# Optimization experiments

Measured on AMD Instinct MI355X. Metric: run time of the kernel, lower is better.

## Reference

```python
import jax, jax.numpy as jnp
import numpy as np

EMB_DIM = 1024
N_HEADS = 16
HEAD_DIM = EMB_DIM // N_HEADS


def setup_inputs() -> dict:
    key = jax.random.key(0)
    ks = jax.random.split(key, 6)
    B, S, D = 2, 2048, EMB_DIM
    s = 1.0 / np.sqrt(D)
    return {
        "x": jax.random.normal(ks[0], (B, S, D), dtype=jnp.float32),
        "wq": jax.random.normal(ks[1], (D, D), dtype=jnp.float32) * s,
        "wk": jax.random.normal(ks[2], (D, D), dtype=jnp.float32) * s,
        "wv": jax.random.normal(ks[3], (D, D), dtype=jnp.float32) * s,
        "wo": jax.random.normal(ks[4], (D, D), dtype=jnp.float32) * s,
        "bo": jax.random.normal(ks[5], (D,), dtype=jnp.float32) * 0.01,
    }


def reference(x, wq, wk, wv, wo, bo):
    B, S, D = x.shape
    H, Hd = N_HEADS, HEAD_DIM
    # projections (torch Linear: y = x @ W.T; here weights are stored as [in, out])
    q = (x @ wq).reshape(B, S, H, Hd).transpose(0, 2, 1, 3)  # [B,H,S,Hd]
    k = (x @ wk).reshape(B, S, H, Hd).transpose(0, 2, 1, 3)
    v = (x @ wv).reshape(B, S, H, Hd).transpose(0, 2, 1, 3)
    scores = jnp.einsum("bhqd,bhkd->bhqk", q, k)  # [B,H,S,S]
    causal = jnp.tril(jnp.ones((S, S), dtype=bool))  # keep lower triangle
    scores = jnp.where(causal, scores, -jnp.inf)
    weights = jax.nn.softmax(scores / np.sqrt(Hd), axis=-1)
    ctx = jnp.einsum("bhqk,bhkd->bhqd", weights, v)  # [B,H,S,Hd]
    ctx = ctx.transpose(0, 2, 1, 3).reshape(B, S, D)
    return ctx @ wo + bo
```

## Files before the change

### kernel.cpp

```cpp
#include <hip/hip_runtime.h>
#include <hip/hip_bf16.h>

constexpr int B = 2, S = 2048, D = 1024, H = 16, Hd = 64;
constexpr int M = B * S;
constexpr int K = 1024;

typedef __attribute__((ext_vector_type(8))) short short8;
typedef __attribute__((ext_vector_type(4))) float f32x4;

__device__ __forceinline__ float bf2f(unsigned short u) {
    return __uint_as_float(((unsigned)u) << 16);
}
__device__ __forceinline__ unsigned short f2bf(float f) {
    unsigned u = __float_as_uint(f);
    u += 0x7FFF + ((u >> 16) & 1);
    return (unsigned short)(u >> 16);
}
__device__ __forceinline__ void gload_lds16(const unsigned short* g, unsigned short* l) {
    __builtin_amdgcn_global_load_lds(
        (const __attribute__((address_space(1))) void*)g,
        (__attribute__((address_space(3))) void*)l, 16, 0, 0);
}

__global__ __launch_bounds__(256) void convert_x_kernel(
    const float* __restrict__ x, unsigned short* __restrict__ xb)
{
    const size_t i = ((size_t)blockIdx.x * 256 + threadIdx.x) * 8;
    float4 a = *(const float4*)(x + i), b = *(const float4*)(x + i + 4);
    ushort4 u0 = {f2bf(a.x), f2bf(a.y), f2bf(a.z), f2bf(a.w)};
    ushort4 u1 = {f2bf(b.x), f2bf(b.y), f2bf(b.z), f2bf(b.w)};
    *(ushort4*)(xb + i) = u0;
    *(ushort4*)(xb + i + 4) = u1;
}

__global__ __launch_bounds__(256) void transpose_w_kernel(
    const float* __restrict__ wq, const float* __restrict__ wk,
    const float* __restrict__ wv, const float* __restrict__ wo,
    unsigned short* __restrict__ wqkv_t, unsigned short* __restrict__ wo_t)
{
    __shared__ float tile[64][65];
    const int z = blockIdx.z;
    const float* w = (z == 0) ? wq : (z == 1) ? wk : (z == 2) ? wv : wo;
    unsigned short* dst = (z == 3) ? wo_t : wqkv_t + (size_t)z * K * K;
    const int k0 = blockIdx.x * 64, n0 = blockIdx.y * 64;
    const int t = threadIdx.x;
    #pragma unroll
    for (int it = 0; it < 16; ++it) {
        int idx = t + it * 256;
        tile[idx >> 6][idx & 63] = w[(size_t)(k0 + (idx >> 6)) * K + n0 + (idx & 63)];
    }
    __syncthreads();
    #pragma unroll
    for (int it = 0; it < 16; ++it) {
        int idx = t + it * 256;
        int r = idx >> 6, c = idx & 63;
        dst[(size_t)(n0 + r) * K + k0 + c] = f2bf(tile[c][r]);
    }
}

__global__ __launch_bounds__(256) void qkv_mfma_kernel(
    const unsigned short* __restrict__ xa, const unsigned short* __restrict__ bt,
    unsigned short* __restrict__ q, unsigned short* __restrict__ k,
    unsigned short* __restrict__ vt)
{
    __shared__ unsigned short A_lds[128][32];
    __shared__ unsigned short B_lds[128][32];
    const int t = threadIdx.x, w = t >> 6, l = t & 63;
    const int lr = l & 15, lg = l >> 4;
    const int wm = w >> 1, wn = w & 1;
    const int m0 = blockIdx.x * 128, n0 = blockIdx.y * 128;
    const int srow = l >> 2, skofs = (l & 3) * 8;

    f32x4 acc[4][4];
    #pragma unroll
    for (int i = 0; i < 4; ++i)
        #pragma unroll
        for (int j = 0; j < 4; ++j) acc[i][j] = (f32x4){0.f, 0.f, 0.f, 0.f};

    for (int k0 = 0; k0 < K; k0 += 32) {
        #pragma unroll
        for (int p = 0; p < 2; ++p) {
            const int c = w * 2 + p;
            gload_lds16(xa + (size_t)(m0 + c * 16 + srow) * K + k0 + skofs, &A_lds[c * 16][0]);
            gload_lds16(bt + (size_t)(n0 + c * 16 + srow) * K + k0 + skofs, &B_lds[c * 16][0]);
        }
        __syncthreads();
        short8 af[4], bf[4];
        #pragma unroll
        for (int i = 0; i < 4; ++i) af[i] = *(const short8*)&A_lds[wm * 64 + i * 16 + lr][lg * 8];
        #pragma unroll
        for (int j = 0; j < 4; ++j) bf[j] = *(const short8*)&B_lds[wn * 64 + j * 16 + lr][lg * 8];
        #pragma unroll
        for (int i = 0; i < 4; ++i)
            #pragma unroll
            for (int j = 0; j < 4; ++j)
                acc[i][j] = __builtin_amdgcn_mfma_f32_16x16x32_bf16(af[i], bf[j], acc[i][j], 0, 0, 0);
        __syncthreads();
    }

    const int z = (n0 >> 10);
    const float scale = (z == 0) ? 0.125f * 1.44269504f : 1.0f;
    #pragma unroll
    for (int i = 0; i < 4; ++i) {
        const int mbase = m0 + wm * 64 + i * 16 + lg * 4;
        #pragma unroll
        for (int j = 0; j < 4; ++j) {
            const int n = n0 + wn * 64 + j * 16 + lr;
            const int nn = n & 1023, hh = nn >> 6, hd = nn & 63;
            #pragma unroll
            for (int r = 0; r < 4; ++r) {
                const int mm = mbase + r, bb = mm >> 11, ss = mm & (S - 1);
                const unsigned short val = f2bf(acc[i][j][r] * scale);
                if (z == 0)      q[((size_t)(bb * H + hh) * S + ss) * Hd + hd] = val;
                else if (z == 1) k[((size_t)(bb * H + hh) * S + ss) * Hd + hd] = val;
                else             vt[((size_t)(bb * H + hh) * Hd + hd) * S + ss] = val;
            }
        }
    }
}

__global__ __launch_bounds__(256) void out_mfma_kernel(
    const unsigned short* __restrict__ a, const unsigned short* __restrict__ bt,
    const float* __restrict__ bias, float* __restrict__ out)
{
    __shared__ unsigned short A_lds[128][32];
    __shared__ unsigned short B_lds[128][32];
    const int t = threadIdx.x, w = t >> 6, l = t & 63;
    const int lr = l & 15, lg = l >> 4;
    const int wm = w >> 1, wn = w & 1;
    const int m0 = blockIdx.x * 128, n0 = blockIdx.y * 128;
    const int srow = l >> 2, skofs = (l & 3) * 8;

    f32x4 acc[4][4];
    #pragma unroll
    for (int i = 0; i < 4; ++i)
        #pragma unroll
        for (int j = 0; j < 4; ++j) acc[i][j] = (f32x4){0.f, 0.f, 0.f, 0.f};

    for (int k0 = 0; k0 < K; k0 += 32) {
        #pragma unroll
        for (int p = 0; p < 2; ++p) {
            const int c = w * 2 + p;
            gload_lds16(a  + (size_t)(m0 + c * 16 + srow) * K + k0 + skofs, &A_lds[c * 16][0]);
            gload_lds16(bt + (size_t)(n0 + c * 16 + srow) * K + k0 + skofs, &B_lds[c * 16][0]);
        }
        __syncthreads();
        short8 af[4], bf[4];
        #pragma unroll
        for (int i = 0; i < 4; ++i) af[i] = *(const short8*)&A_lds[wm * 64 + i * 16 + lr][lg * 8];
        #pragma unroll
        for (int j = 0; j < 4; ++j) bf[j] = *(const short8*)&B_lds[wn * 64 + j * 16 + lr][lg * 8];
        #pragma unroll
        for (int i = 0; i < 4; ++i)
            #pragma unroll
            for (int j = 0; j < 4; ++j)
                acc[i][j] = __builtin_amdgcn_mfma_f32_16x16x32_bf16(af[i], bf[j], acc[i][j], 0, 0, 0);
        __syncthreads();
    }

    #pragma unroll
    for (int i = 0; i < 4; ++i) {
        const int mbase = m0 + wm * 64 + i * 16 + lg * 4;
        #pragma unroll
        for (int j = 0; j < 4; ++j) {
            const int n = n0 + wn * 64 + j * 16 + lr;
            const float bv = bias[n];
            #pragma unroll
            for (int r = 0; r < 4; ++r)
                out[(size_t)(mbase + r) * D + n] = acc[i][j][r] + bv;
        }
    }
}

__global__ __launch_bounds__(256) void attn_mfma_kernel(
    const unsigned short* __restrict__ q, const unsigned short* __restrict__ k,
    const unsigned short* __restrict__ vt, unsigned short* __restrict__ ctx)
{
    __shared__ unsigned short Kb[64 * 64];
    __shared__ unsigned short Vb[64 * 64];
    __shared__ unsigned short P_lds[4][16][72];
    const int t = threadIdx.x, w = t >> 6, l = t & 63;
    const int lr = l & 15, lg = l >> 4;
    const int hh = blockIdx.y, bb = blockIdx.z;
    const int qt = ((int)blockIdx.x + 5 * (int)blockIdx.y + 16 * (int)blockIdx.z) & 31;
    const int q0 = qt * 64 + w * 16;
    const int diag = qt;
    const size_t base  = (size_t)(bb * H + hh) * S * Hd;
    const size_t vbase = (size_t)(bb * H + hh) * Hd * S;

    const int srow0 = w * 16 + (l >> 3);
    const int scol  = (l & 7) * 8;

    short8 qf[2];
    #pragma unroll
    for (int c = 0; c < 2; ++c)
        qf[c] = *(const short8*)(q + base + (size_t)(q0 + lr) * Hd + c * 32 + lg * 8);

    f32x4 accO[4];
    #pragma unroll
    for (int hb = 0; hb < 4; ++hb) accO[hb] = (f32x4){0.f, 0.f, 0.f, 0.f};
    float m_run = -INFINITY, l_run = 0.f;

    {
        short8 k0r[2], v0r[2];
        #pragma unroll
        for (int it = 0; it < 2; ++it) {
            const int row = srow0 + it * 8;
            k0r[it] = *(const short8*)(k + base + (size_t)row * Hd + scol);
            v0r[it] = *(const short8*)(vt + vbase + (size_t)row * S + scol);
        }
        #pragma unroll
        for (int it = 0; it < 2; ++it) {
            const int row = srow0 + it * 8;
            const int wc = (scol ^ ((row & 7) * 8));
            *(short8*)&Kb[row * 64 + wc] = k0r[it];
            *(short8*)&Vb[row * 64 + wc] = v0r[it];
        }
    }
    __syncthreads();

    for (int kt = 0; kt <= diag; ++kt) {
        short8 nK[2], nV[2];
        if (kt < diag) {
            const unsigned short* kg = k + base + (size_t)(kt + 1) * 64 * Hd;
            const unsigned short* vg = vt + vbase + (size_t)(kt + 1) * 64;
            #pragma unroll
            for (int it = 0; it < 2; ++it) {
                const int row = srow0 + it * 8;
                nK[it] = *(const short8*)(kg + (size_t)row * Hd + scol);
                nV[it] = *(const short8*)(vg + (size_t)row * S + scol);
            }
        }

        f32x4 accS[4];
        __builtin_amdgcn_s_setprio(1);
        #pragma unroll
        for (int kc = 0; kc < 4; ++kc) {
            accS[kc] = (f32x4){0.f, 0.f, 0.f, 0.f};
            const int krow = kc * 16 + lr;
            #pragma unroll
            for (int c = 0; c < 2; ++c) {
                short8 kf = *(const short8*)&Kb[krow * 64 +
                    ((c * 32 + lg * 8) ^ ((krow & 7) * 8))];
                accS[kc] = __builtin_amdgcn_mfma_f32_16x16x32_bf16(kf, qf[c], accS[kc], 0, 0, 0);
            }
        }
        __builtin_amdgcn_s_setprio(0);

        float ps[16];
        #pragma unroll
        for (int kc = 0; kc < 4; ++kc)
            #pragma unroll
            for (int r = 0; r < 4; ++r) {
                float s = accS[kc][r];
                if (kt == diag && (kc * 16 + lg * 4 + r > w * 16 + lr)) s = -INFINITY;
                ps[kc * 4 + r] = s;
            }
        float m8[8];
        #pragma unroll
        for (int i = 0; i < 8; ++i) m8[i] = fmaxf(ps[i], ps[i + 8]);
        float m4a = fmaxf(m8[0], m8[4]), m4b = fmaxf(m8[1], m8[5]);
        float m4c = fmaxf(m8[2], m8[6]), m4d = fmaxf(m8[3], m8[7]);
        float mloc = fmaxf(fmaxf(m4a, m4b), fmaxf(m4c, m4d));
        mloc = fmaxf(mloc, __shfl_xor(mloc, 16));
        mloc = fmaxf(mloc, __shfl_xor(mloc, 32));

        const bool resc = __any(mloc > m_run + 8.f);
        const float mn = resc ? fmaxf(m_run, mloc) : m_run;

        #pragma unroll
        for (int i = 0; i < 16; ++i) ps[i] = exp2f(ps[i] - mn);
        float s8[8];
        #pragma unroll
        for (int i = 0; i < 8; ++i) s8[i] = ps[i] + ps[i + 8];
        float rs = ((s8[0] + s8[4]) + (s8[1] + s8[5])) +
                   ((s8[2] + s8[6]) + (s8[3] + s8[7]));
        rs += __shfl_xor(rs, 16);
        rs += __shfl_xor(rs, 32);

        if (resc) {
            const float sfc = exp2f(m_run - mn);
            l_run = l_run * sfc + rs;
            m_run = mn;
            #pragma unroll
            for (int hb = 0; hb < 4; ++hb)
                #pragma unroll
                for (int r = 0; r < 4; ++r) accO[hb][r] *= sfc;
        } else {
            l_run += rs;
        }

        #pragma unroll
        for (int kc = 0; kc < 4; ++kc) {
            uint2 pk;
            *(__hip_bfloat162*)&pk.x =
                __float22bfloat162_rn(make_float2(ps[kc * 4 + 0], ps[kc * 4 + 1]));
            *(__hip_bfloat162*)&pk.y =
                __float22bfloat162_rn(make_float2(ps[kc * 4 + 2], ps[kc * 4 + 3]));
            *(uint2*)&P_lds[w][lr][kc * 16 + lg * 4] = pk;
        }
        short8 pa[2];
        #pragma unroll
        for (int c = 0; c < 2; ++c)
            pa[c] = *(const short8*)&P_lds[w][lr][c * 32 + lg * 8];

        __builtin_amdgcn_s_setprio(1);
        #pragma unroll
        for (int hb = 0; hb < 4; ++hb) {
            const int vrow = hb * 16 + lr;
            #pragma unroll
            for (int c = 0; c < 2; ++c) {
                short8 vf = *(const short8*)&Vb[vrow * 64 +
                    ((c * 32 + lg * 8) ^ ((vrow & 7) * 8))];
                accO[hb] = __builtin_amdgcn_mfma_f32_16x16x32_bf16(vf, pa[c], accO[hb], 0, 0, 0);
            }
        }
        __builtin_amdgcn_s_setprio(0);

        __syncthreads();
        if (kt < diag) {
            #pragma unroll
            for (int it = 0; it < 2; ++it) {
                const int row = srow0 + it * 8;
                const int wc = (scol ^ ((row & 7) * 8));
                *(short8*)&Kb[row * 64 + wc] = nK[it];
                *(short8*)&Vb[row * 64 + wc] = nV[it];
            }
            __syncthreads();
        }
    }

    const float inv = 1.f / l_run;
    unsigned short* crow = ctx + (size_t)(bb * S + q0 + lr) * D + hh * Hd + lg * 4;
    #pragma unroll
    for (int hb = 0; hb < 4; ++hb) {
        ushort4 o;
        o.x = f2bf(accO[hb][0] * inv);
        o.y = f2bf(accO[hb][1] * inv);
        o.z = f2bf(accO[hb][2] * inv);
        o.w = f2bf(accO[hb][3] * inv);
        *(ushort4*)(crow + hb * 16) = o;
    }
}

extern "C" void kernel_launch(void* const* d_in, const int* in_sizes, int n_in,
                              void* d_out, int out_size, void* d_ws, size_t ws_size,
                              hipStream_t stream) {
    const float* x  = (const float*)d_in[0];
    const float* wq = (const float*)d_in[1];
    const float* wk = (const float*)d_in[2];
    const float* wv = (const float*)d_in[3];
    const float* wo = (const float*)d_in[4];
    const float* bo = (const float*)d_in[5];
    float* out = (float*)d_out;

    char* ws = (char*)d_ws;
    unsigned short* x_bf   = (unsigned short*)ws;
    unsigned short* q      = (unsigned short*)(ws + ((size_t)8  << 20));
    unsigned short* kk     = (unsigned short*)(ws + ((size_t)16 << 20));
    unsigned short* vt     = (unsigned short*)(ws + ((size_t)24 << 20));
    unsigned short* ctx    = x_bf;
    unsigned short* wqkv_t = (unsigned short*)(ws + ((size_t)32 << 20));
    unsigned short* wo_t   = (unsigned short*)(ws + ((size_t)38 << 20));

    convert_x_kernel<<<(M * K) / (256 * 8), 256, 0, stream>>>(x, x_bf);
    dim3 gtr(K / 64, K / 64, 4);
    transpose_w_kernel<<<gtr, 256, 0, stream>>>(wq, wk, wv, wo, wqkv_t, wo_t);

    dim3 gqkv(M / 128, 3072 / 128);
    qkv_mfma_kernel<<<gqkv, 256, 0, stream>>>(x_bf, wqkv_t, q, kk, vt);

    dim3 gattn(S / 64, H, B);
    attn_mfma_kernel<<<gattn, 256, 0, stream>>>(q, kk, vt, ctx);

    dim3 gout(M / 128, D / 128);
    out_mfma_kernel<<<gout, 256, 0, stream>>>(ctx, wo_t, bo, out);
}
```

Before: 132.7 us.

## Double-buffer GEMM LDS tiles and remap attention blocks to XCDs

Both projection GEMM kernels now use two LDS buffers and issue the async global-to-LDS loads for the next K slice before computing on the current one. This removes one barrier per iteration and is meant to hide load latency. The attention launch becomes a 1D grid whose block index is decoded so that all blocks of a given batch-head land on the same XCD, improving L2 reuse of K/V. Query tiles alternate forward and reverse order to balance the causal workload. LDS use in the GEMMs doubles, which may reduce occupancy.

Result: no change. 130.9 us (-1.3%).

```diff
diff --git a/kernel.cpp b/kernel.cpp
--- a/kernel.cpp
+++ b/kernel.cpp
@@ -63,8 +63,8 @@
     unsigned short* __restrict__ q, unsigned short* __restrict__ k,
     unsigned short* __restrict__ vt)
 {
-    __shared__ unsigned short A_lds[128][32];
-    __shared__ unsigned short B_lds[128][32];
+    __shared__ unsigned short A_lds[2][128][32];
+    __shared__ unsigned short B_lds[2][128][32];
     const int t = threadIdx.x, w = t >> 6, l = t & 63;
     const int lr = l & 15, lg = l >> 4;
     const int wm = w >> 1, wn = w & 1;
@@ -77,25 +77,38 @@
         #pragma unroll
         for (int j = 0; j < 4; ++j) acc[i][j] = (f32x4){0.f, 0.f, 0.f, 0.f};
 
+    #pragma unroll
+    for (int p = 0; p < 2; ++p) {
+        const int c = w * 2 + p;
+        gload_lds16(xa + (size_t)(m0 + c * 16 + srow) * K + skofs, &A_lds[0][c * 16][0]);
+        gload_lds16(bt + (size_t)(n0 + c * 16 + srow) * K + skofs, &B_lds[0][c * 16][0]);
+    }
+    __syncthreads();
+
+    int cur = 0;
     for (int k0 = 0; k0 < K; k0 += 32) {
-        #pragma unroll
-        for (int p = 0; p < 2; ++p) {
-            const int c = w * 2 + p;
-            gload_lds16(xa + (size_t)(m0 + c * 16 + srow) * K + k0 + skofs, &A_lds[c * 16][0]);
-            gload_lds16(bt + (size_t)(n0 + c * 16 + srow) * K + k0 + skofs, &B_lds[c * 16][0]);
-        }
-        __syncthreads();
+        if (k0 + 32 < K) {
+            #pragma unroll
+            for (int p = 0; p < 2; ++p) {
+                const int c = w * 2 + p;
+                gload_lds16(xa + (size_t)(m0 + c * 16 + srow) * K + k0 + 32 + skofs,
+                            &A_lds[cur ^ 1][c * 16][0]);
+                gload_lds16(bt + (size_t)(n0 + c * 16 + srow) * K + k0 + 32 + skofs,
+                            &B_lds[cur ^ 1][c * 16][0]);
+            }
+        }
         short8 af[4], bf[4];
         #pragma unroll
-        for (int i = 0; i < 4; ++i) af[i] = *(const short8*)&A_lds[wm * 64 + i * 16 + lr][lg * 8];
-        #pragma unroll
-        for (int j = 0; j < 4; ++j) bf[j] = *(const short8*)&B_lds[wn * 64 + j * 16 + lr][lg * 8];
+        for (int i = 0; i < 4; ++i) af[i] = *(const short8*)&A_lds[cur][wm * 64 + i * 16 + lr][lg * 8];
+        #pragma unroll
+        for (int j = 0; j < 4; ++j) bf[j] = *(const short8*)&B_lds[cur][wn * 64 + j * 16 + lr][lg * 8];
         #pragma unroll
         for (int i = 0; i < 4; ++i)
             #pragma unroll
             for (int j = 0; j < 4; ++j)
                 acc[i][j] = __builtin_amdgcn_mfma_f32_16x16x32_bf16(af[i], bf[j], acc[i][j], 0, 0, 0);
         __syncthreads();
+        cur ^= 1;
     }
 
     const int z = (n0 >> 10);
@@ -123,8 +136,8 @@
     const unsigned short* __restrict__ a, const unsigned short* __restrict__ bt,
     const float* __restrict__ bias, float* __restrict__ out)
 {
-    __shared__ unsigned short A_lds[128][32];
-    __shared__ unsigned short B_lds[128][32];
+    __shared__ unsigned short A_lds[2][128][32];
+    __shared__ unsigned short B_lds[2][128][32];
     const int t = threadIdx.x, w = t >> 6, l = t & 63;
     const int lr = l & 15, lg = l >> 4;
     const int wm = w >> 1, wn = w & 1;
@@ -137,25 +150,38 @@
         #pragma unroll
         for (int j = 0; j < 4; ++j) acc[i][j] = (f32x4){0.f, 0.f, 0.f, 0.f};
 
+    #pragma unroll
+    for (int p = 0; p < 2; ++p) {
+        const int c = w * 2 + p;
+        gload_lds16(a  + (size_t)(m0 + c * 16 + srow) * K + skofs, &A_lds[0][c * 16][0]);
+        gload_lds16(bt + (size_t)(n0 + c * 16 + srow) * K + skofs, &B_lds[0][c * 16][0]);
+    }
+    __syncthreads();
+
+    int cur = 0;
     for (int k0 = 0; k0 < K; k0 += 32) {
-        #pragma unroll
-        for (int p = 0; p < 2; ++p) {
-            const int c = w * 2 + p;
-            gload_lds16(a  + (size_t)(m0 + c * 16 + srow) * K + k0 + skofs, &A_lds[c * 16][0]);
-            gload_lds16(bt + (size_t)(n0 + c * 16 + srow) * K + k0 + skofs, &B_lds[c * 16][0]);
-        }
-        __syncthreads();
+        if (k0 + 32 < K) {
+            #pragma unroll
+            for (int p = 0; p < 2; ++p) {
+                const int c = w * 2 + p;
+                gload_lds16(a  + (size_t)(m0 + c * 16 + srow) * K + k0 + 32 + skofs,
+                            &A_lds[cur ^ 1][c * 16][0]);
+                gload_lds16(bt + (size_t)(n0 + c * 16 + srow) * K + k0 + 32 + skofs,
+                            &B_lds[cur ^ 1][c * 16][0]);
+            }
+        }
         short8 af[4], bf[4];
         #pragma unroll
-        for (int i = 0; i < 4; ++i) af[i] = *(const short8*)&A_lds[wm * 64 + i * 16 + lr][lg * 8];
-        #pragma unroll
-        for (int j = 0; j < 4; ++j) bf[j] = *(const short8*)&B_lds[wn * 64 + j * 16 + lr][lg * 8];
+        for (int i = 0; i < 4; ++i) af[i] = *(const short8*)&A_lds[cur][wm * 64 + i * 16 + lr][lg * 8];
+        #pragma unroll
+        for (int j = 0; j < 4; ++j) bf[j] = *(const short8*)&B_lds[cur][wn * 64 + j * 16 + lr][lg * 8];
         #pragma unroll
         for (int i = 0; i < 4; ++i)
             #pragma unroll
             for (int j = 0; j < 4; ++j)
                 acc[i][j] = __builtin_amdgcn_mfma_f32_16x16x32_bf16(af[i], bf[j], acc[i][j], 0, 0, 0);
         __syncthreads();
+        cur ^= 1;
     }
 
     #pragma unroll
@@ -181,8 +207,16 @@
     __shared__ unsigned short P_lds[4][16][72];
     const int t = threadIdx.x, w = t >> 6, l = t & 63;
     const int lr = l & 15, lg = l >> 4;
-    const int hh = blockIdx.y, bb = blockIdx.z;
-    const int qt = ((int)blockIdx.x + 5 * (int)blockIdx.y + 16 * (int)blockIdx.z) & 31;
+
+    const int bid = blockIdx.x;
+    const int xcd = bid & 7;
+    const int j   = bid >> 3;
+    const int m   = j >> 5;
+    const int c   = j & 31;
+    const int bh  = xcd * 4 + m;
+    const int bb  = bh >> 4, hh = bh & 15;
+    const int qt  = (m & 1) ? (31 - c) : c;
+
     const int q0 = qt * 64 + w * 16;
     const int diag = qt;
     const size_t base  = (size_t)(bb * H + hh) * S * Hd;
@@ -193,8 +227,8 @@
 
     short8 qf[2];
     #pragma unroll
-    for (int c = 0; c < 2; ++c)
-        qf[c] = *(const short8*)(q + base + (size_t)(q0 + lr) * Hd + c * 32 + lg * 8);
+    for (int cc = 0; cc < 2; ++cc)
+        qf[cc] = *(const short8*)(q + base + (size_t)(q0 + lr) * Hd + cc * 32 + lg * 8);
 
     f32x4 accO[4];
     #pragma unroll
@@ -239,10 +273,10 @@
             accS[kc] = (f32x4){0.f, 0.f, 0.f, 0.f};
             const int krow = kc * 16 + lr;
             #pragma unroll
-            for (int c = 0; c < 2; ++c) {
+            for (int cc = 0; cc < 2; ++cc) {
                 short8 kf = *(const short8*)&Kb[krow * 64 +
-                    ((c * 32 + lg * 8) ^ ((krow & 7) * 8))];
-                accS[kc] = __builtin_amdgcn_mfma_f32_16x16x32_bf16(kf, qf[c], accS[kc], 0, 0, 0);
+                    ((cc * 32 + lg * 8) ^ ((krow & 7) * 8))];
+                accS[kc] = __builtin_amdgcn_mfma_f32_16x16x32_bf16(kf, qf[cc], accS[kc], 0, 0, 0);
             }
         }
         __builtin_amdgcn_s_setprio(0);
@@ -301,18 +335,18 @@
         }
         short8 pa[2];
         #pragma unroll
-        for (int c = 0; c < 2; ++c)
-            pa[c] = *(const short8*)&P_lds[w][lr][c * 32 + lg * 8];
+        for (int cc = 0; cc < 2; ++cc)
+            pa[cc] = *(const short8*)&P_lds[w][lr][cc * 32 + lg * 8];
 
         __builtin_amdgcn_s_setprio(1);
         #pragma unroll
         for (int hb = 0; hb < 4; ++hb) {
             const int vrow = hb * 16 + lr;
             #pragma unroll
-            for (int c = 0; c < 2; ++c) {
+            for (int cc = 0; cc < 2; ++cc) {
                 short8 vf = *(const short8*)&Vb[vrow * 64 +
-                    ((c * 32 + lg * 8) ^ ((vrow & 7) * 8))];
-                accO[hb] = __builtin_amdgcn_mfma_f32_16x16x32_bf16(vf, pa[c], accO[hb], 0, 0, 0);
+                    ((cc * 32 + lg * 8) ^ ((vrow & 7) * 8))];
+                accO[hb] = __builtin_amdgcn_mfma_f32_16x16x32_bf16(vf, pa[cc], accO[hb], 0, 0, 0);
             }
         }
         __builtin_amdgcn_s_setprio(0);
@@ -370,8 +404,7 @@
     dim3 gqkv(M / 128, 3072 / 128);
     qkv_mfma_kernel<<<gqkv, 256, 0, stream>>>(x_bf, wqkv_t, q, kk, vt);
 
-    dim3 gattn(S / 64, H, B);
-    attn_mfma_kernel<<<gattn, 256, 0, stream>>>(q, kk, vt, ctx);
+    attn_mfma_kernel<<<1024, 256, 0, stream>>>(q, kk, vt, ctx);
 
     dim3 gout(M / 128, D / 128);
     out_mfma_kernel<<<gout, 256, 0, stream>>>(ctx, wo_t, bo, out);
```
